# Performance work log

Hardware: AMD Instinct MI355X
Metric: run time of the kernel (lower is better)

The kernel has to match this reference:

```python
import jax, jax.numpy as jnp
import numpy as np

W_BIT = 4
OUT_F = 11008
IN_F = 4096
K = 16


def unpack_sign(q_bytes):
    """q_bytes: [n_bytes] int32 holding uint8 values. Little-endian bit order.
    Returns float32 signs in {-1, +1} of shape [OUT_F, IN_F]."""
    bits = (q_bytes[:, None] >> jnp.arange(8, dtype=q_bytes.dtype)) & 1  # [n_bytes, 8]
    signs = (2 * bits - 1).astype(jnp.float32)
    return signs.reshape(OUT_F, IN_F)


def setup_inputs() -> dict:
    key = jax.random.key(0)
    k0, k1, k2, k3 = jax.random.split(key, 4)
    x = jax.random.normal(k0, (4, 2048, IN_F), dtype=jnp.float32)
    # packed sign bits: one byte stores 8 signs; OUT_F*IN_F//8 bytes per bit-plane
    qweight = jax.random.randint(k1, (W_BIT, OUT_F * IN_F // 8), 0, 256, dtype=jnp.int32)
    u = jax.random.normal(k2, (W_BIT, OUT_F, K), dtype=jnp.float32) * 0.05
    vt = jax.random.normal(k3, (W_BIT, K, IN_F), dtype=jnp.float32) * 0.05
    return {"x": x, "qweight": qweight, "u": u, "vt": vt}


def reference(x, qweight, u, vt):
    # Reconstruct full weight: w = sum_i sign_i * (u_i @ vt_i), then GEMM x @ w.T.
    # Loop over the small fixed w_bit count to avoid holding all [OUT,IN] bit-planes at once.
    w = jnp.zeros((OUT_F, IN_F), dtype=x.dtype)
    for i in range(W_BIT):
        signs = unpack_sign(qweight[i])            # [OUT_F, IN_F]
        w = w + signs * (u[i] @ vt[i])             # rank-K reconstruction masked by signs
    return x @ w.T                                  # [B, S, OUT_F]
```

## Files before the change

kernel.cpp:

```cpp
#include <hip/hip_runtime.h>
#include <hip/hip_bf16.h>

#define W_BIT 4
#define OUT_F 11008
#define IN_F 4096
#define KRANK 16
#define M_DIM 8192
#define QW_PLANE (OUT_F * IN_F / 8)

#define N_DIM OUT_F
#define K_DIM 4096
#define NT 64
#define NBN 43

typedef __attribute__((ext_vector_type(8))) short short8;
typedef __attribute__((ext_vector_type(4))) float f32x4;

__device__ __forceinline__ short f2bf(float f) {
    union { float f; unsigned u; } v;
    v.f = f;
    unsigned r = v.u + 0x7fffu + ((v.u >> 16) & 1u);
    return (short)(r >> 16);
}

__device__ __forceinline__ void async16(void* lds_p, const void* g) {
    __builtin_amdgcn_global_load_lds(
        (const __attribute__((address_space(1))) unsigned int*)g,
        (__attribute__((address_space(3))) unsigned int*)lds_p,
        16, 0, 0);
}

#define BAR() __builtin_amdgcn_s_barrier()
#define LGKM0() do { asm volatile("s_waitcnt lgkmcnt(0)" ::: "memory"); \
                     __builtin_amdgcn_sched_barrier(0); } while (0)
#define VMC(n) do { asm volatile("s_waitcnt vmcnt(" #n ")" ::: "memory"); \
                    __builtin_amdgcn_sched_barrier(0); } while (0)
#define PRIO1() __builtin_amdgcn_s_setprio(1)
#define PRIO0() __builtin_amdgcn_s_setprio(0)

__global__ __launch_bounds__(256) void convert_x_kernel(
    const float* __restrict__ x, short* __restrict__ xb) {
    int tid = blockIdx.x * blockDim.x + threadIdx.x;
    int stride = gridDim.x * blockDim.x;
    const int n8 = (M_DIM * IN_F) / 8;
    for (int i = tid; i < n8; i += stride) {
        f32x4 a = ((const f32x4*)x)[2 * i];
        f32x4 b = ((const f32x4*)x)[2 * i + 1];
        short8 o;
        o[0] = f2bf(a[0]); o[1] = f2bf(a[1]); o[2] = f2bf(a[2]); o[3] = f2bf(a[3]);
        o[4] = f2bf(b[0]); o[5] = f2bf(b[1]); o[6] = f2bf(b[2]); o[7] = f2bf(b[3]);
        ((short8*)xb)[i] = o;
    }
}

__global__ __launch_bounds__(256) void reconstruct_w_kernel(
    const int* __restrict__ qw, const float* __restrict__ u,
    const float* __restrict__ vt, short* __restrict__ wb) {
    __shared__ float vts[W_BIT][KRANK][128];
    __shared__ float us[W_BIT][KRANK][64];

    const int t = threadIdx.x;
    const int o0 = blockIdx.y * 64;
    const int c0 = blockIdx.x * 128;

    for (int idx = t; idx < W_BIT * KRANK * 128; idx += 256) {
        int i = idx >> 11;
        int rem = idx & 2047;
        int k = rem >> 7;
        int c = rem & 127;
        vts[i][k][c] = vt[(i * KRANK + k) * IN_F + c0 + c];
    }
    for (int idx = t; idx < W_BIT * KRANK * 64; idx += 256) {
        int i = idx >> 10;
        int rem = idx & 1023;
        int o = rem >> 4;
        int k = rem & 15;
        us[i][k][o] = u[((size_t)i * OUT_F + o0 + o) * KRANK + k];
    }
    __syncthreads();

    const int to = (t >> 4) * 4;
    const int tc = (t & 15) * 8;

    float wacc[4][8];
#pragma unroll
    for (int r = 0; r < 4; ++r)
#pragma unroll
        for (int c = 0; c < 8; ++c) wacc[r][c] = 0.f;

#pragma unroll
    for (int i = 0; i < W_BIT; ++i) {
        float dot[4][8];
#pragma unroll
        for (int r = 0; r < 4; ++r)
#pragma unroll
            for (int c = 0; c < 8; ++c) dot[r][c] = 0.f;

#pragma unroll
        for (int k = 0; k < KRANK; ++k) {
            f32x4 uv = *(const f32x4*)&us[i][k][to];
            f32x4 v0 = *(const f32x4*)&vts[i][k][tc];
            f32x4 v1 = *(const f32x4*)&vts[i][k][tc + 4];
#pragma unroll
            for (int r = 0; r < 4; ++r) {
#pragma unroll
                for (int c = 0; c < 4; ++c) {
                    dot[r][c]     += uv[r] * v0[c];
                    dot[r][c + 4] += uv[r] * v1[c];
                }
            }
        }
#pragma unroll
        for (int r = 0; r < 4; ++r) {
            unsigned byte = (unsigned)qw[i * QW_PLANE + (((o0 + to + r) * IN_F + c0 + tc) >> 3)];
#pragma unroll
            for (int c = 0; c < 8; ++c) {
                wacc[r][c] += ((byte >> c) & 1u) ? dot[r][c] : -dot[r][c];
            }
        }
    }

#pragma unroll
    for (int r = 0; r < 4; ++r) {
        short8 o8;
#pragma unroll
        for (int c = 0; c < 8; ++c) o8[c] = f2bf(wacc[r][c]);
        *(short8*)&wb[(size_t)(o0 + to + r) * IN_F + c0 + tc] = o8;
    }
}

__global__ __launch_bounds__(512, 2) void gemm256_kernel(
    const short* __restrict__ A, const short* __restrict__ B, float* __restrict__ C) {
    extern __shared__ short lds[];

    const int t = threadIdx.x;
    const int lane = t & 63, wid = t >> 6;
    const int wr = wid >> 2, wc = wid & 3;
    const int fr = lane & 15, fq = lane >> 4;

    const int bid = blockIdx.x;
    const int cpx = gridDim.x >> 3;
    const int swzb = (bid & 7) * cpx + (bid >> 3);
    const int bm = swzb / NBN, bn = swzb % NBN;
    const long row0 = (long)bm * 256, col0 = (long)bn * 256;

    const int colswz = (fq ^ ((fr >> 1) & 3)) * 8;
    const int aoff = (wr * 128 + fr) * 32 + colswz;
    const int boff = 32768 + (wc * 64 + fr) * 32 + colswz;

    const int srow = t >> 2;
    const int sswz = (((t & 3) ^ ((srow >> 1) & 3)) << 3);
    const short* pA0 = A + (row0 + srow) * (size_t)K_DIM + sswz;
    const short* pA1 = pA0 + (size_t)128 * K_DIM;
    const short* pB0 = B + (col0 + srow) * (size_t)K_DIM + sswz;
    const short* pB1 = pB0 + (size_t)128 * K_DIM;
    const int ldst0 = t * 8;

    f32x4 acc[8][4];
#pragma unroll
    for (int m = 0; m < 8; ++m)
#pragma unroll
        for (int n = 0; n < 4; ++n) acc[m][n] = (f32x4)0.f;

    short8 af[4], bf0[4], bf1[4];

#define STG(P0, P1, SLOT, OFFB) do {                                   \
    async16(&lds[(SLOT) + ldst0], (const char*)(P0) + (OFFB));         \
    async16(&lds[(SLOT) + 4096 + ldst0], (const char*)(P1) + (OFFB));  \
} while (0)

#define RDA(KSLOT, MH) do {                                            \
    _Pragma("unroll") for (int m = 0; m < 4; ++m)                      \
        af[m] = *(const short8*)&lds[(KSLOT) + ((MH) * 4 + m) * 512 + aoff]; \
} while (0)

#define RDB(DST, KSLOT) do {                                           \
    _Pragma("unroll") for (int n = 0; n < 4; ++n)                      \
        DST[n] = *(const short8*)&lds[(KSLOT) + n * 512 + boff];       \
} while (0)

#define MFQ(BF, MH) do {                                               \
    _Pragma("unroll") for (int m = 0; m < 4; ++m)                      \
        _Pragma("unroll") for (int n = 0; n < 4; ++n)                  \
            acc[(MH) * 4 + m][n] = __builtin_amdgcn_mfma_f32_16x16x32_bf16( \
                af[m], BF[n], acc[(MH) * 4 + m][n], 0, 0, 0);          \
} while (0)

#define MMA(BF, MH) do { PRIO1(); MFQ(BF, MH); PRIO0(); } while (0)

    STG(pA0, pA1, 0,     0);
    STG(pB0, pB1, 32768, 0);
    STG(pA0, pA1, 8192,  64);
    STG(pB0, pB1, 40960, 64);
    STG(pA0, pA1, 16384, 128);
    STG(pB0, pB1, 49152, 128);
    VMC(8);
    BAR();

    for (int it = 0; it < 31; ++it) {
        RDB(bf0, 0); RDA(0, 0);
        STG(pA0, pA1, 24576, 192);
        BAR(); LGKM0(); MMA(bf0, 0); BAR();
        RDA(0, 1);
        VMC(6);
        STG(pB0, pB1, 57344, 192);
        BAR(); LGKM0(); MMA(bf0, 1); BAR();
        RDB(bf1, 8192); RDA(8192, 0);
        STG(pA0, pA1, 0, 256);
        BAR(); LGKM0(); MMA(bf1, 0); BAR();
        RDA(8192, 1);
        VMC(6);
        STG(pB0, pB1, 32768, 256);
        BAR(); LGKM0(); MMA(bf1, 1); BAR();

        RDB(bf0, 16384); RDA(16384, 0);
        STG(pA0, pA1, 8192, 320);
        BAR(); LGKM0(); MMA(bf0, 0); BAR();
        RDA(16384, 1);
        VMC(6);
        STG(pB0, pB1, 40960, 320);
        BAR(); LGKM0(); MMA(bf0, 1); BAR();
        RDB(bf1, 24576); RDA(24576, 0);
        STG(pA0, pA1, 16384, 384);
        BAR(); LGKM0(); MMA(bf1, 0); BAR();
        RDA(24576, 1);
        VMC(6);
        STG(pB0, pB1, 49152, 384);
        BAR(); LGKM0(); MMA(bf1, 1); BAR();

        pA0 += 128; pA1 += 128; pB0 += 128; pB1 += 128;
    }

    RDB(bf0, 0); RDA(0, 0);
    STG(pA0, pA1, 24576, 192);
    BAR(); LGKM0(); MMA(bf0, 0); BAR();
    RDA(0, 1);
    VMC(2);
    STG(pB0, pB1, 57344, 192);
    BAR(); LGKM0(); MMA(bf0, 1); BAR();
    RDB(bf1, 8192); RDA(8192, 0);
    BAR(); LGKM0(); MMA(bf1, 0); BAR();
    RDA(8192, 1);
    VMC(0);
    BAR(); LGKM0(); MMA(bf1, 1); BAR();
    RDB(bf0, 16384); RDA(16384, 0);
    BAR(); LGKM0(); MMA(bf0, 0); BAR();
    RDA(16384, 1);
    BAR(); LGKM0(); MMA(bf0, 1); BAR();
    RDB(bf1, 24576); RDA(24576, 0);
    BAR(); LGKM0(); MMA(bf1, 0); BAR();
    RDA(24576, 1);
    BAR(); LGKM0(); MMA(bf1, 1); BAR();

#pragma unroll
    for (int m = 0; m < 8; ++m) {
#pragma unroll
        for (int n = 0; n < 4; ++n) {
            f32x4 v = acc[m][n];
            long r0 = row0 + wr * 128 + m * 16 + fq * 4;
            long cc = col0 + wc * 64 + n * 16 + fr;
#pragma unroll
            for (int jj = 0; jj < 4; ++jj)
                C[(size_t)(r0 + jj) * N_DIM + cc] = v[jj];
        }
    }
#undef STG
#undef RDA
#undef RDB
#undef MFQ
#undef MMA
}

extern "C" void kernel_launch(void* const* d_in, const int* in_sizes, int n_in,
                              void* d_out, int out_size, void* d_ws, size_t ws_size,
                              hipStream_t stream) {
    const float* x  = (const float*)d_in[0];
    const int*   qw = (const int*)d_in[1];
    const float* u  = (const float*)d_in[2];
    const float* vt = (const float*)d_in[3];
    float* out = (float*)d_out;

    const size_t wb_bytes = (size_t)OUT_F * IN_F * 2;
    short* wb = (short*)d_ws;
    short* xb = (short*)((char*)d_ws + wb_bytes);

    (void)hipFuncSetAttribute((const void*)gemm256_kernel,
                              hipFuncAttributeMaxDynamicSharedMemorySize, 131072);

    hipLaunchKernelGGL(convert_x_kernel, dim3(2048), dim3(256), 0, stream, x, xb);
    hipLaunchKernelGGL(reconstruct_w_kernel, dim3(IN_F / 128, OUT_F / 64), dim3(256), 0, stream,
                       qw, u, vt, wb);
    hipLaunchKernelGGL(gemm256_kernel, dim3((M_DIM / 256) * (N_DIM / 256)), dim3(512), 131072,
                       stream, xb, wb, out);
}
```

Before: 904.7 us.

## Switch GEMM inner loop from 16x16x32 to 32x32x16 bf16 MFMA

```diff
diff --git a/kernel.cpp b/kernel.cpp
--- a/kernel.cpp
+++ b/kernel.cpp
@@ -15,6 +15,7 @@
 
 typedef __attribute__((ext_vector_type(8))) short short8;
 typedef __attribute__((ext_vector_type(4))) float f32x4;
+typedef __attribute__((ext_vector_type(16))) float f32x16;
 
 __device__ __forceinline__ short f2bf(float f) {
     union { float f; unsigned u; } v;
@@ -136,7 +137,7 @@
     const int t = threadIdx.x;
     const int lane = t & 63, wid = t >> 6;
     const int wr = wid >> 2, wc = wid & 3;
-    const int fr = lane & 15, fq = lane >> 4;
+    const int lr = lane & 31, lh = lane >> 5;
 
     const int bid = blockIdx.x;
     const int cpx = gridDim.x >> 3;
@@ -144,9 +145,11 @@
     const int bm = swzb / NBN, bn = swzb % NBN;
     const long row0 = (long)bm * 256, col0 = (long)bn * 256;
 
-    const int colswz = (fq ^ ((fr >> 1) & 3)) * 8;
-    const int aoff = (wr * 128 + fr) * 32 + colswz;
-    const int boff = 32768 + (wc * 64 + fr) * 32 + colswz;
+    const int lswz = (lr >> 1) & 3;
+    const int acol0 = ((lh) ^ lswz) * 8;
+    const int acol1 = ((2 | lh) ^ lswz) * 8;
+    const int abase = (wr * 128 + lr) * 32;
+    const int bbase = 32768 + (wc * 64 + lr) * 32;
 
     const int srow = t >> 2;
     const int sswz = (((t & 3) ^ ((srow >> 1) & 3)) << 3);
@@ -156,37 +159,34 @@
     const short* pB1 = pB0 + (size_t)128 * K_DIM;
     const int ldst0 = t * 8;
 
-    f32x4 acc[8][4];
-#pragma unroll
-    for (int m = 0; m < 8; ++m)
-#pragma unroll
-        for (int n = 0; n < 4; ++n) acc[m][n] = (f32x4)0.f;
-
-    short8 af[4], bf0[4], bf1[4];
+    f32x16 acc[4][2];
+#pragma unroll
+    for (int m = 0; m < 4; ++m)
+#pragma unroll
+        for (int n = 0; n < 2; ++n) acc[m][n] = (f32x16)0.f;
+
+    short8 af[4], bf[2];
 
 #define STG(P0, P1, SLOT, OFFB) do {                                   \
     async16(&lds[(SLOT) + ldst0], (const char*)(P0) + (OFFB));         \
     async16(&lds[(SLOT) + 4096 + ldst0], (const char*)(P1) + (OFFB));  \
 } while (0)
 
-#define RDA(KSLOT, MH) do {                                            \
+#define RD6(KSLOT, COL) do {                                           \
+    _Pragma("unroll") for (int n = 0; n < 2; ++n)                      \
+        bf[n] = *(const short8*)&lds[(KSLOT) + bbase + n * 1024 + (COL)]; \
     _Pragma("unroll") for (int m = 0; m < 4; ++m)                      \
-        af[m] = *(const short8*)&lds[(KSLOT) + ((MH) * 4 + m) * 512 + aoff]; \
+        af[m] = *(const short8*)&lds[(KSLOT) + abase + m * 1024 + (COL)]; \
 } while (0)
 
-#define RDB(DST, KSLOT) do {                                           \
-    _Pragma("unroll") for (int n = 0; n < 4; ++n)                      \
-        DST[n] = *(const short8*)&lds[(KSLOT) + n * 512 + boff];       \
+#define MMA8() do {                                                    \
+    PRIO1();                                                           \
+    _Pragma("unroll") for (int m = 0; m < 4; ++m)                      \
+        _Pragma("unroll") for (int n = 0; n < 2; ++n)                  \
+            acc[m][n] = __builtin_amdgcn_mfma_f32_32x32x16_bf16(       \
+                af[m], bf[n], acc[m][n], 0, 0, 0);                     \
+    PRIO0();                                                           \
 } while (0)
-
-#define MFQ(BF, MH) do {                                               \
-    _Pragma("unroll") for (int m = 0; m < 4; ++m)                      \
-        _Pragma("unroll") for (int n = 0; n < 4; ++n)                  \
-            acc[(MH) * 4 + m][n] = __builtin_amdgcn_mfma_f32_16x16x32_bf16( \
-                af[m], BF[n], acc[(MH) * 4 + m][n], 0, 0, 0);          \
-} while (0)
-
-#define MMA(BF, MH) do { PRIO1(); MFQ(BF, MH); PRIO0(); } while (0)
 
     STG(pA0, pA1, 0,     0);
     STG(pB0, pB1, 32768, 0);
@@ -198,77 +198,77 @@
     BAR();
 
     for (int it = 0; it < 31; ++it) {
-        RDB(bf0, 0); RDA(0, 0);
+        RD6(0, acol0);
         STG(pA0, pA1, 24576, 192);
-        BAR(); LGKM0(); MMA(bf0, 0); BAR();
-        RDA(0, 1);
+        BAR(); LGKM0(); MMA8(); BAR();
+        RD6(0, acol1);
         VMC(6);
         STG(pB0, pB1, 57344, 192);
-        BAR(); LGKM0(); MMA(bf0, 1); BAR();
-        RDB(bf1, 8192); RDA(8192, 0);
+        BAR(); LGKM0(); MMA8(); BAR();
+        RD6(8192, acol0);
         STG(pA0, pA1, 0, 256);
-        BAR(); LGKM0(); MMA(bf1, 0); BAR();
-        RDA(8192, 1);
+        BAR(); LGKM0(); MMA8(); BAR();
+        RD6(8192, acol1);
         VMC(6);
         STG(pB0, pB1, 32768, 256);
-        BAR(); LGKM0(); MMA(bf1, 1); BAR();
-
-        RDB(bf0, 16384); RDA(16384, 0);
+        BAR(); LGKM0(); MMA8(); BAR();
+
+        RD6(16384, acol0);
         STG(pA0, pA1, 8192, 320);
-        BAR(); LGKM0(); MMA(bf0, 0); BAR();
-        RDA(16384, 1);
+        BAR(); LGKM0(); MMA8(); BAR();
+        RD6(16384, acol1);
         VMC(6);
         STG(pB0, pB1, 40960, 320);
-        BAR(); LGKM0(); MMA(bf0, 1); BAR();
-        RDB(bf1, 24576); RDA(24576, 0);
+        BAR(); LGKM0(); MMA8(); BAR();
+        RD6(24576, acol0);
         STG(pA0, pA1, 16384, 384);
-        BAR(); LGKM0(); MMA(bf1, 0); BAR();
-        RDA(24576, 1);
+        BAR(); LGKM0(); MMA8(); BAR();
+        RD6(24576, acol1);
         VMC(6);
         STG(pB0, pB1, 49152, 384);
-        BAR(); LGKM0(); MMA(bf1, 1); BAR();
+        BAR(); LGKM0(); MMA8(); BAR();
 
         pA0 += 128; pA1 += 128; pB0 += 128; pB1 += 128;
     }
 
-    RDB(bf0, 0); RDA(0, 0);
+    RD6(0, acol0);
     STG(pA0, pA1, 24576, 192);
-    BAR(); LGKM0(); MMA(bf0, 0); BAR();
-    RDA(0, 1);
+    BAR(); LGKM0(); MMA8(); BAR();
+    RD6(0, acol1);
     VMC(2);
     STG(pB0, pB1, 57344, 192);
-    BAR(); LGKM0(); MMA(bf0, 1); BAR();
-    RDB(bf1, 8192); RDA(8192, 0);
-    BAR(); LGKM0(); MMA(bf1, 0); BAR();
-    RDA(8192, 1);
+    BAR(); LGKM0(); MMA8(); BAR();
+    RD6(8192, acol0);
+    BAR(); LGKM0(); MMA8(); BAR();
+    RD6(8192, acol1);
     VMC(0);
-    BAR(); LGKM0(); MMA(bf1, 1); BAR();
-    RDB(bf0, 16384); RDA(16384, 0);
-    BAR(); LGKM0(); MMA(bf0, 0); BAR();
-    RDA(16384, 1);
-    BAR(); LGKM0(); MMA(bf0, 1); BAR();
-    RDB(bf1, 24576); RDA(24576, 0);
-    BAR(); LGKM0(); MMA(bf1, 0); BAR();
-    RDA(24576, 1);
-    BAR(); LGKM0(); MMA(bf1, 1); BAR();
-
-#pragma unroll
-    for (int m = 0; m < 8; ++m) {
-#pragma unroll
-        for (int n = 0; n < 4; ++n) {
-            f32x4 v = acc[m][n];
-            long r0 = row0 + wr * 128 + m * 16 + fq * 4;
-            long cc = col0 + wc * 64 + n * 16 + fr;
-#pragma unroll
-            for (int jj = 0; jj < 4; ++jj)
-                C[(size_t)(r0 + jj) * N_DIM + cc] = v[jj];
+    BAR(); LGKM0(); MMA8(); BAR();
+    RD6(16384, acol0);
+    BAR(); LGKM0(); MMA8(); BAR();
+    RD6(16384, acol1);
+    BAR(); LGKM0(); MMA8(); BAR();
+    RD6(24576, acol0);
+    BAR(); LGKM0(); MMA8(); BAR();
+    RD6(24576, acol1);
+    BAR(); LGKM0(); MMA8(); BAR();
+
+#pragma unroll
+    for (int m = 0; m < 4; ++m) {
+#pragma unroll
+        for (int n = 0; n < 2; ++n) {
+            f32x16 v = acc[m][n];
+            long cc = col0 + wc * 64 + n * 32 + lr;
+            long rb = row0 + wr * 128 + m * 32 + 4 * lh;
+#pragma unroll
+            for (int reg = 0; reg < 16; ++reg) {
+                long r = rb + (reg & 3) + 8 * (reg >> 2);
+                C[(size_t)r * N_DIM + cc] = v[reg];
+            }
         }
     }
 #undef STG
-#undef RDA
-#undef RDB
-#undef MFQ
-#undef MMA
+#undef RD6
+#undef MMA8
 }
 
 extern "C" void kernel_launch(void* const* d_in, const int* in_sizes, int n_in,
```

Measured after the change: 957.3 us. 1.06x slower.

## Halve GEMM barriers per phase and batch global-load waits per half-iteration

Applied to the files above, without the earlier changes.

```diff
diff --git a/kernel.cpp b/kernel.cpp
--- a/kernel.cpp
+++ b/kernel.cpp
@@ -64,17 +64,11 @@
     const int c0 = blockIdx.x * 128;
 
     for (int idx = t; idx < W_BIT * KRANK * 128; idx += 256) {
-        int i = idx >> 11;
-        int rem = idx & 2047;
-        int k = rem >> 7;
-        int c = rem & 127;
+        int i = idx >> 11, rem = idx & 2047, k = rem >> 7, c = rem & 127;
         vts[i][k][c] = vt[(i * KRANK + k) * IN_F + c0 + c];
     }
     for (int idx = t; idx < W_BIT * KRANK * 64; idx += 256) {
-        int i = idx >> 10;
-        int rem = idx & 1023;
-        int o = rem >> 4;
-        int k = rem & 15;
+        int i = idx >> 10, rem = idx & 1023, o = rem >> 4, k = rem & 15;
         us[i][k][o] = u[((size_t)i * OUT_F + o0 + o) * KRANK + k];
     }
     __syncthreads();
@@ -95,7 +89,6 @@
         for (int r = 0; r < 4; ++r)
 #pragma unroll
             for (int c = 0; c < 8; ++c) dot[r][c] = 0.f;
-
 #pragma unroll
         for (int k = 0; k < KRANK; ++k) {
             f32x4 uv = *(const f32x4*)&us[i][k][to];
@@ -114,12 +107,10 @@
         for (int r = 0; r < 4; ++r) {
             unsigned byte = (unsigned)qw[i * QW_PLANE + (((o0 + to + r) * IN_F + c0 + tc) >> 3)];
 #pragma unroll
-            for (int c = 0; c < 8; ++c) {
+            for (int c = 0; c < 8; ++c)
                 wacc[r][c] += ((byte >> c) & 1u) ? dot[r][c] : -dot[r][c];
-            }
         }
     }
-
 #pragma unroll
     for (int r = 0; r < 4; ++r) {
         short8 o8;
@@ -186,7 +177,8 @@
                 af[m], BF[n], acc[(MH) * 4 + m][n], 0, 0, 0);          \
 } while (0)
 
-#define MMA(BF, MH) do { PRIO1(); MFQ(BF, MH); PRIO0(); } while (0)
+#define MMA(BF, MH) do { PRIO1(); MFQ(BF, MH); PRIO0();                \
+    __builtin_amdgcn_sched_barrier(0); } while (0)
 
     STG(pA0, pA1, 0,     0);
     STG(pB0, pB1, 32768, 0);
@@ -194,63 +186,60 @@
     STG(pB0, pB1, 40960, 64);
     STG(pA0, pA1, 16384, 128);
     STG(pB0, pB1, 49152, 128);
-    VMC(8);
+    VMC(4);
     BAR();
 
     for (int it = 0; it < 31; ++it) {
         RDB(bf0, 0); RDA(0, 0);
         STG(pA0, pA1, 24576, 192);
-        BAR(); LGKM0(); MMA(bf0, 0); BAR();
+        BAR(); LGKM0(); MMA(bf0, 0);
         RDA(0, 1);
-        VMC(6);
         STG(pB0, pB1, 57344, 192);
-        BAR(); LGKM0(); MMA(bf0, 1); BAR();
+        BAR(); LGKM0(); MMA(bf0, 1);
         RDB(bf1, 8192); RDA(8192, 0);
         STG(pA0, pA1, 0, 256);
-        BAR(); LGKM0(); MMA(bf1, 0); BAR();
+        BAR(); LGKM0(); MMA(bf1, 0);
         RDA(8192, 1);
-        VMC(6);
         STG(pB0, pB1, 32768, 256);
-        BAR(); LGKM0(); MMA(bf1, 1); BAR();
+        VMC(4);
+        BAR(); LGKM0(); MMA(bf1, 1);
 
         RDB(bf0, 16384); RDA(16384, 0);
         STG(pA0, pA1, 8192, 320);
-        BAR(); LGKM0(); MMA(bf0, 0); BAR();
+        BAR(); LGKM0(); MMA(bf0, 0);
         RDA(16384, 1);
-        VMC(6);
         STG(pB0, pB1, 40960, 320);
-        BAR(); LGKM0(); MMA(bf0, 1); BAR();
+        BAR(); LGKM0(); MMA(bf0, 1);
         RDB(bf1, 24576); RDA(24576, 0);
         STG(pA0, pA1, 16384, 384);
-        BAR(); LGKM0(); MMA(bf1, 0); BAR();
+        BAR(); LGKM0(); MMA(bf1, 0);
         RDA(24576, 1);
-        VMC(6);
         STG(pB0, pB1, 49152, 384);
-        BAR(); LGKM0(); MMA(bf1, 1); BAR();
+        VMC(4);
+        BAR(); LGKM0(); MMA(bf1, 1);
 
         pA0 += 128; pA1 += 128; pB0 += 128; pB1 += 128;
     }
 
     RDB(bf0, 0); RDA(0, 0);
     STG(pA0, pA1, 24576, 192);
-    BAR(); LGKM0(); MMA(bf0, 0); BAR();
+    BAR(); LGKM0(); MMA(bf0, 0);
     RDA(0, 1);
-    VMC(2);
     STG(pB0, pB1, 57344, 192);
-    BAR(); LGKM0(); MMA(bf0, 1); BAR();
+    BAR(); LGKM0(); MMA(bf0, 1);
     RDB(bf1, 8192); RDA(8192, 0);
-    BAR(); LGKM0(); MMA(bf1, 0); BAR();
+    BAR(); LGKM0(); MMA(bf1, 0);
     RDA(8192, 1);
     VMC(0);
-    BAR(); LGKM0(); MMA(bf1, 1); BAR();
+    BAR(); LGKM0(); MMA(bf1, 1);
     RDB(bf0, 16384); RDA(16384, 0);
-    BAR(); LGKM0(); MMA(bf0, 0); BAR();
+    BAR(); LGKM0(); MMA(bf0, 0);
     RDA(16384, 1);
-    BAR(); LGKM0(); MMA(bf0, 1); BAR();
+    BAR(); LGKM0(); MMA(bf0, 1);
     RDB(bf1, 24576); RDA(24576, 0);
-    BAR(); LGKM0(); MMA(bf1, 0); BAR();
+    BAR(); LGKM0(); MMA(bf1, 0);
     RDA(24576, 1);
-    BAR(); LGKM0(); MMA(bf1, 1); BAR();
+    BAR(); LGKM0(); MMA(bf1, 1);
 
 #pragma unroll
     for (int m = 0; m < 8; ++m) {
```

After: 881.7 us. -2.5%, faster.
